# Kernel optimization log

Measured on AMD Instinct MI355X. Metric: run time of the kernel, lower is better.

The kernel has to match this reference:

```python
import jax, jax.numpy as jnp
import numpy as np

K_MASK = -2.3819763e+38
NUM_KV_HEADS = 4
SOFT_CAP = 50.0
WINDOW = 1024
ROPE_BASE = 10000.0
ROPE_SCALE = 1.0


def rms_norm(x, scale=None, eps=1e-6):
    var = jnp.mean(jnp.square(x), axis=-1, keepdims=True)
    normed = x * jax.lax.rsqrt(var + eps)
    if scale is not None:
        normed = normed * (1.0 + scale)
    return normed


def apply_rope(x, positions):
    # x: [B, T, N, H], positions: [B, T]
    head_dim = x.shape[-1]
    fraction = 2.0 * jnp.arange(head_dim // 2, dtype=jnp.float32) / head_dim
    timescale = ROPE_BASE ** fraction  # [H/2]
    sinusoid = positions[..., None, None].astype(jnp.float32) / timescale / ROPE_SCALE  # [B,T,1,H/2]
    sin, cos = jnp.sin(sinusoid), jnp.cos(sinusoid)
    first, second = jnp.split(x, 2, axis=-1)
    return jnp.concatenate([first * cos - second * sin,
                            second * cos + first * sin], axis=-1).astype(x.dtype)


def setup_inputs() -> dict:
    key = jax.random.key(0)
    ks = jax.random.split(key, 8)
    B, T, D, N, K, H, F = 2, 2048, 2048, 8, NUM_KV_HEADS, 256, 8192
    CACHE = 4096
    x = jax.random.normal(ks[0], (B, T, D), dtype=jnp.float32)
    segment_pos = jnp.broadcast_to(jnp.arange(T, dtype=jnp.int32)[None, :], (B, T))
    # causal mask over cache slots: after scatter, slot s (< T) holds position s; slots >= T are empty
    s_idx = jnp.arange(CACHE)
    t_idx = jnp.arange(T)
    attn_mask = (s_idx[None, :] <= t_idx[:, None]) & (s_idx[None, :] < T)
    attn_mask = jnp.broadcast_to(attn_mask[None], (B, T, CACHE))
    cache_k = jnp.zeros((B, CACHE, K, H), dtype=jnp.float32)
    cache_v = jnp.zeros((B, CACHE, K, H), dtype=jnp.float32)
    cache_positions = jnp.zeros((B, CACHE), dtype=jnp.int32)
    end_index = jnp.zeros((B,), dtype=jnp.int32)
    w_q = jax.random.normal(ks[1], (N, D, H), dtype=jnp.float32) * 0.02
    w_kv = jax.random.normal(ks[2], (2, K, D, H), dtype=jnp.float32) * 0.02
    w_attn_vec = jax.random.normal(ks[3], (N, H, D), dtype=jnp.float32) * 0.02
    w_gating = jax.random.normal(ks[4], (2, F, D), dtype=jnp.float32) * 0.02
    w_linear = jax.random.normal(ks[5], (F, D), dtype=jnp.float32) * 0.02
    return {
        'x': x, 'segment_pos': segment_pos, 'attn_mask': attn_mask,
        'cache_k': cache_k, 'cache_v': cache_v,
        'cache_positions': cache_positions, 'end_index': end_index,
        'w_q': w_q, 'w_kv': w_kv, 'w_attn_vec': w_attn_vec,
        'q_norm_scale': jnp.zeros((H,), dtype=jnp.float32),
        'k_norm_scale': jnp.zeros((H,), dtype=jnp.float32),
        'pre_attn_scale': jnp.zeros((D,), dtype=jnp.float32),
        'post_attn_scale': jnp.zeros((D,), dtype=jnp.float32),
        'pre_ffw_scale': jnp.zeros((D,), dtype=jnp.float32),
        'post_ffw_scale': jnp.zeros((D,), dtype=jnp.float32),
        'w_gating': w_gating, 'w_linear': w_linear,
        'skip_scale': jnp.ones((1,), dtype=jnp.float32),
    }


def reference(x, segment_pos, attn_mask, cache_k, cache_v, cache_positions, end_index,
              w_q, w_kv, w_attn_vec, q_norm_scale, k_norm_scale,
              pre_attn_scale, post_attn_scale, pre_ffw_scale, post_ffw_scale,
              w_gating, w_linear, skip_scale):
    B, T, D = x.shape
    cache_size = cache_v.shape[1]

    h = rms_norm(x, pre_attn_scale)

    # --- attention ---
    q = jnp.einsum('BTD,NDH->BTNH', h, w_q)
    q = rms_norm(q, q_norm_scale)
    q = apply_rope(q, segment_pos)

    k, v = jnp.einsum('BSD,CKDH->CBSKH', h, w_kv)
    k = rms_norm(k, k_norm_scale)
    v = rms_norm(v, None)
    k = apply_rope(k, segment_pos)

    # KV-cache scatter (ring-buffer indexing)
    idx = (end_index[:, None] + jnp.arange(T)[None, :]) % cache_size  # [B,T]
    bidx = jnp.arange(B)[:, None]
    v = cache_v.at[bidx, idx].set(v)              # [B,S,K,H]
    k = cache_k.at[bidx, idx].set(k)
    cache_pos = cache_positions.at[bidx, idx].set(segment_pos)  # [B,S]

    # GQA logits
    N, H = q.shape[2], q.shape[3]
    G = N // NUM_KV_HEADS
    qg = q.reshape(B, T, NUM_KV_HEADS, G, H)
    logits = jnp.einsum('BTKGH,BSKH->BTKGS', qg, k).reshape(B, T, N, cache_size)

    # soft cap
    logits = jnp.tanh(logits / SOFT_CAP) * SOFT_CAP

    # sliding-window mask against cache positions
    sliding = (cache_pos[:, None, :] > segment_pos[:, :, None] - WINDOW) & \
              (cache_pos[:, None, :] < segment_pos[:, :, None] + WINDOW)  # [B,T,S]
    mask = attn_mask & sliding

    padded = jnp.where(mask[:, :, None, :], logits, K_MASK)
    probs = jax.nn.softmax(padded, axis=-1).astype(k.dtype)

    pg = probs.reshape(B, T, NUM_KV_HEADS, G, cache_size)
    encoded = jnp.einsum('BTKGS,BSKH->BTKGH', pg, v).reshape(B, T, N, H)
    attn_out = jnp.einsum('BTNH,NHD->BTD', encoded, w_attn_vec)

    # post-attn norm + residual (skip_scale on the skip connection)
    attn_out = rms_norm(attn_out, post_attn_scale)
    attn_out = x * skip_scale + attn_out

    # --- feed-forward ---
    ffw_in = rms_norm(attn_out, pre_ffw_scale)
    gate = jnp.einsum('BTF,CHF->BTCH', ffw_in, w_gating)  # C=2
    act = jax.nn.gelu(gate[..., 0, :]) * gate[..., 1, :]
    ffw_out = jnp.einsum('BTH,HF->BTF', act, w_linear)
    ffw_out = rms_norm(ffw_out, post_ffw_scale)

    return attn_out + ffw_out
```

## Files before the change

kernel.cpp:

```cpp
#include <hip/hip_runtime.h>


typedef _Float16 h8 __attribute__((ext_vector_type(8)));
typedef _Float16 h4 __attribute__((ext_vector_type(4)));
typedef float f4 __attribute__((ext_vector_type(4)));

#define BDIM 2
#define TDIM 2048
#define DDIM 2048
#define NQ 8
#define NKV 4
#define HDIM 256
#define FDIM 8192
#define MROWS (BDIM * TDIM)
#define WINDOW 1024
#define QS 4096

#define BAR() asm volatile("s_barrier" ::: "memory")

__device__ __forceinline__ float gelu_fast(float x) {
  float u = 1.5957691216057308f * (x + 0.044715f * x * x * x);
  float e = __expf(u);
  return x * e / (e + 1.f);
}

__device__ __forceinline__ void g2l16(const _Float16* g, _Float16* l) {
  __builtin_amdgcn_global_load_lds(
      (const __attribute__((address_space(1))) void*)g,
      (__attribute__((address_space(3))) void*)l, 16, 0, 0);
}

__device__ inline float block_sum(float v, float* sbuf) {
#pragma unroll
  for (int off = 32; off; off >>= 1) v += __shfl_xor(v, off, 64);
  __syncthreads();
  if ((threadIdx.x & 63) == 0) sbuf[threadIdx.x >> 6] = v;
  __syncthreads();
  return sbuf[0] + sbuf[1] + sbuf[2] + sbuf[3];
}

template <int EPI>
__global__ __launch_bounds__(512, 2) void gemm256(
    const _Float16* __restrict__ A, const _Float16* __restrict__ Bt,
    void* __restrict__ Cout, int M, int Nc, int K) {
  __shared__ _Float16 As[3][256 * 64];
  __shared__ _Float16 Bs[3][128 * 64];
  (void)M;
  const int tid = threadIdx.x;
  const int lane = tid & 63, w = tid >> 6;
  const int nwg = gridDim.x;
  const int bid2 = (blockIdx.x & 7) * (nwg >> 3) + (blockIdx.x >> 3);
  const int nbx = Nc >> 7;
  const int bx = bid2 % nbx, by = bid2 / nbx;
  const int m0 = by * 256, n0 = bx * 128;
  const int wm = (w >> 1) * 64, wn = (w & 1) * 64;
  const int l16 = lane & 15, quad = lane >> 4;

  const int lr = lane >> 3;
  const int swz8 = ((lane & 7) ^ lr) << 3;
  const _Float16* Ag = A + (size_t)(m0 + w * 32 + lr) * K + swz8;
  const _Float16* Bg = Bt + (size_t)(n0 + w * 16 + lr) * K + swz8;

  const int qs8 = (quad ^ (l16 & 3)) << 3;
  const int kxo = ((l16 >> 2) & 1) << 5;
  int aoff[4], boff[4];
#pragma unroll
  for (int i = 0; i < 4; i++) {
    aoff[i] = (wm + i * 16 + l16) * 64 + qs8;
    boff[i] = (wn + i * 16 + l16) * 64 + qs8;
  }

  f4 acc[4][4];
#pragma unroll
  for (int i = 0; i < 4; i++)
#pragma unroll
    for (int j = 0; j < 4; j++) {
      acc[i][j][0] = 0.f; acc[i][j][1] = 0.f; acc[i][j][2] = 0.f; acc[i][j][3] = 0.f;
    }

#define SA(b, kt, c) g2l16(Ag + (size_t)(c) * 8 * K + (size_t)(kt) * 64, \
                           &As[b][(w * 32 + (c) * 8) * 64])
#define SB(b, kt, c) g2l16(Bg + (size_t)(c) * 8 * K + (size_t)(kt) * 64, \
                           &Bs[b][(w * 16 + (c) * 8) * 64])

  SA(0, 0, 0); SA(0, 0, 1); SA(0, 0, 2); SA(0, 0, 3); SB(0, 0, 0); SB(0, 0, 1);
  SA(1, 1, 0); SA(1, 1, 1); SA(1, 1, 2); SA(1, 1, 3); SB(1, 1, 0); SB(1, 1, 1);
  asm volatile("s_waitcnt vmcnt(6)" ::: "memory");
  BAR();

  const int nt = K >> 6;
  for (int kt = 0; kt < nt; ++kt) {
    const int cur = kt % 3, nb = (kt + 2) % 3;
    const bool pf = (kt + 2) < nt;
    const _Float16* Ab = As[cur];
    const _Float16* Bb = Bs[cur];
    h8 af[4][2], bf[4][2];
#pragma unroll
    for (int i = 0; i < 4; i++) {
      af[i][0] = *(const h8*)&Ab[aoff[i] + kxo];
      af[i][1] = *(const h8*)&Ab[aoff[i] + (kxo ^ 32)];
    }
#pragma unroll
    for (int i = 0; i < 2; i++) {
      bf[i][0] = *(const h8*)&Bb[boff[i] + kxo];
      bf[i][1] = *(const h8*)&Bb[boff[i] + (kxo ^ 32)];
    }
    if (pf) { SA(nb, kt + 2, 0); SA(nb, kt + 2, 1); SA(nb, kt + 2, 2); }
    BAR();
    __builtin_amdgcn_s_setprio(1);
#pragma unroll
    for (int mi = 0; mi < 4; mi++)
#pragma unroll
      for (int ni = 0; ni < 2; ni++)
#pragma unroll
        for (int ks = 0; ks < 2; ks++)
          acc[mi][ni] = __builtin_amdgcn_mfma_f32_16x16x32_f16(
              af[mi][ks], bf[ni][ks], acc[mi][ni], 0, 0, 0);
    __builtin_amdgcn_s_setprio(0);
    BAR();
#pragma unroll
    for (int i = 2; i < 4; i++) {
      bf[i][0] = *(const h8*)&Bb[boff[i] + kxo];
      bf[i][1] = *(const h8*)&Bb[boff[i] + (kxo ^ 32)];
    }
    if (pf) { SA(nb, kt + 2, 3); SB(nb, kt + 2, 0); SB(nb, kt + 2, 1); }
    BAR();
    __builtin_amdgcn_s_setprio(1);
#pragma unroll
    for (int mi = 0; mi < 4; mi++)
#pragma unroll
      for (int ni = 2; ni < 4; ni++)
#pragma unroll
        for (int ks = 0; ks < 2; ks++)
          acc[mi][ni] = __builtin_amdgcn_mfma_f32_16x16x32_f16(
              af[mi][ks], bf[ni][ks], acc[mi][ni], 0, 0, 0);
    __builtin_amdgcn_s_setprio(0);
    if (pf)                 asm volatile("s_waitcnt vmcnt(6)" ::: "memory");
    else if (kt + 2 == nt)  asm volatile("s_waitcnt vmcnt(0)" ::: "memory");
    BAR();
  }
#undef SA
#undef SB

#pragma unroll
  for (int mi = 0; mi < 4; mi++)
#pragma unroll
    for (int ni = 0; ni < 4; ni++)
#pragma unroll
      for (int r = 0; r < 4; r++) {
        const int rg = m0 + wm + mi * 16 + quad * 4 + r;
        const int cg = n0 + wn + ni * 16 + l16;
        const size_t idx = (size_t)rg * Nc + cg;
        if (EPI == 0) ((float*)Cout)[idx] = acc[mi][ni][r];
        else          ((_Float16*)Cout)[idx] = (_Float16)acc[mi][ni][r];
      }
}

__global__ __launch_bounds__(512, 2) void gemm_gate256(
    const _Float16* __restrict__ A, const _Float16* __restrict__ B0,
    const _Float16* __restrict__ B1, _Float16* __restrict__ act,
    int M, int Nc, int K) {
  __shared__ _Float16 As[3][256 * 64];
  __shared__ _Float16 B0s[3][64 * 64];
  __shared__ _Float16 B1s[3][64 * 64];
  (void)M;
  const int tid = threadIdx.x;
  const int lane = tid & 63, w = tid >> 6;
  const int nwg = gridDim.x;
  const int bid2 = (blockIdx.x & 7) * (nwg >> 3) + (blockIdx.x >> 3);
  const int nbx = Nc >> 6;
  const int bx = bid2 % nbx, by = bid2 / nbx;
  const int m0 = by * 256, n0 = bx * 64;
  const int wm = (w >> 1) * 64, wn = (w & 1) * 32;
  const int l16 = lane & 15, quad = lane >> 4;

  const int lr = lane >> 3;
  const int swz8 = ((lane & 7) ^ lr) << 3;
  const _Float16* Ag  = A  + (size_t)(m0 + w * 32 + lr) * K + swz8;
  const _Float16* B0g = B0 + (size_t)(n0 + w * 8 + lr) * K + swz8;
  const _Float16* B1g = B1 + (size_t)(n0 + w * 8 + lr) * K + swz8;

  const int qs8 = (quad ^ (l16 & 3)) << 3;
  const int kxo = ((l16 >> 2) & 1) << 5;
  int aoff[4], boff[2];
#pragma unroll
  for (int i = 0; i < 4; i++) aoff[i] = (wm + i * 16 + l16) * 64 + qs8;
#pragma unroll
  for (int i = 0; i < 2; i++) boff[i] = (wn + i * 16 + l16) * 64 + qs8;

  f4 acc0[4][2], acc1[4][2];
#pragma unroll
  for (int i = 0; i < 4; i++)
#pragma unroll
    for (int j = 0; j < 2; j++) {
      acc0[i][j][0] = 0.f; acc0[i][j][1] = 0.f; acc0[i][j][2] = 0.f; acc0[i][j][3] = 0.f;
      acc1[i][j][0] = 0.f; acc1[i][j][1] = 0.f; acc1[i][j][2] = 0.f; acc1[i][j][3] = 0.f;
    }

#define SA(b, kt, c) g2l16(Ag + (size_t)(c) * 8 * K + (size_t)(kt) * 64, \
                           &As[b][(w * 32 + (c) * 8) * 64])
#define SB0(b, kt) g2l16(B0g + (size_t)(kt) * 64, &B0s[b][w * 8 * 64])
#define SB1(b, kt) g2l16(B1g + (size_t)(kt) * 64, &B1s[b][w * 8 * 64])

  SA(0, 0, 0); SA(0, 0, 1); SA(0, 0, 2); SA(0, 0, 3); SB0(0, 0); SB1(0, 0);
  SA(1, 1, 0); SA(1, 1, 1); SA(1, 1, 2); SA(1, 1, 3); SB0(1, 1); SB1(1, 1);
  asm volatile("s_waitcnt vmcnt(6)" ::: "memory");
  BAR();

  const int nt = K >> 6;
  for (int kt = 0; kt < nt; ++kt) {
    const int cur = kt % 3, nb = (kt + 2) % 3;
    const bool pf = (kt + 2) < nt;
    const _Float16* Ab = As[cur];
    const _Float16* Bb0 = B0s[cur];
    const _Float16* Bb1 = B1s[cur];
    h8 af[4][2], b0f[2][2], b1f[2][2];
#pragma unroll
    for (int i = 0; i < 4; i++) {
      af[i][0] = *(const h8*)&Ab[aoff[i] + kxo];
      af[i][1] = *(const h8*)&Ab[aoff[i] + (kxo ^ 32)];
    }
#pragma unroll
    for (int i = 0; i < 2; i++) {
      b0f[i][0] = *(const h8*)&Bb0[boff[i] + kxo];
      b0f[i][1] = *(const h8*)&Bb0[boff[i] + (kxo ^ 32)];
    }
    if (pf) { SA(nb, kt + 2, 0); SA(nb, kt + 2, 1); SA(nb, kt + 2, 2); }
    BAR();
    __builtin_amdgcn_s_setprio(1);
#pragma unroll
    for (int mi = 0; mi < 4; mi++)
#pragma unroll
      for (int ni = 0; ni < 2; ni++)
#pragma unroll
        for (int ks = 0; ks < 2; ks++)
          acc0[mi][ni] = __builtin_amdgcn_mfma_f32_16x16x32_f16(
              af[mi][ks], b0f[ni][ks], acc0[mi][ni], 0, 0, 0);
    __builtin_amdgcn_s_setprio(0);
    BAR();
#pragma unroll
    for (int i = 0; i < 2; i++) {
      b1f[i][0] = *(const h8*)&Bb1[boff[i] + kxo];
      b1f[i][1] = *(const h8*)&Bb1[boff[i] + (kxo ^ 32)];
    }
    if (pf) { SA(nb, kt + 2, 3); SB0(nb, kt + 2); SB1(nb, kt + 2); }
    BAR();
    __builtin_amdgcn_s_setprio(1);
#pragma unroll
    for (int mi = 0; mi < 4; mi++)
#pragma unroll
      for (int ni = 0; ni < 2; ni++)
#pragma unroll
        for (int ks = 0; ks < 2; ks++)
          acc1[mi][ni] = __builtin_amdgcn_mfma_f32_16x16x32_f16(
              af[mi][ks], b1f[ni][ks], acc1[mi][ni], 0, 0, 0);
    __builtin_amdgcn_s_setprio(0);
    if (pf)                 asm volatile("s_waitcnt vmcnt(6)" ::: "memory");
    else if (kt + 2 == nt)  asm volatile("s_waitcnt vmcnt(0)" ::: "memory");
    BAR();
  }
#undef SA
#undef SB0
#undef SB1

#pragma unroll
  for (int mi = 0; mi < 4; mi++)
#pragma unroll
    for (int ni = 0; ni < 2; ni++)
#pragma unroll
      for (int r = 0; r < 4; r++) {
        const int rg = m0 + wm + mi * 16 + quad * 4 + r;
        const int cg = n0 + wn + ni * 16 + l16;
        act[(size_t)rg * Nc + cg] =
            (_Float16)(gelu_fast(acc0[mi][ni][r]) * acc1[mi][ni][r]);
      }
}

__global__ __launch_bounds__(256) void transpose_cast_kernel(
    const float* __restrict__ in, _Float16* __restrict__ out,
    int R, int C, size_t in_zstride, size_t out_zstride) {
  __shared__ float tile[64][65];
  const float* ip = in + blockIdx.z * in_zstride;
  _Float16* op = out + blockIdx.z * out_zstride;
  const int cb = blockIdx.x * 64, rb = blockIdx.y * 64;
  const int tx = threadIdx.x & 15, ty = threadIdx.x >> 4;
#pragma unroll
  for (int i = 0; i < 4; i++) {
    f4 v = *(const f4*)&ip[(size_t)(rb + ty + 16 * i) * C + cb + tx * 4];
    tile[ty + 16 * i][tx * 4 + 0] = v[0];
    tile[ty + 16 * i][tx * 4 + 1] = v[1];
    tile[ty + 16 * i][tx * 4 + 2] = v[2];
    tile[ty + 16 * i][tx * 4 + 3] = v[3];
  }
  __syncthreads();
#pragma unroll
  for (int i = 0; i < 4; i++) {
    const int c = ty + 16 * i;
    h4 o;
#pragma unroll
    for (int j = 0; j < 4; j++) o[j] = (_Float16)tile[tx * 4 + j][c];
    *(h4*)&op[(size_t)(cb + c) * R + rb + tx * 4] = o;
  }
}

__global__ void cast_fp16_kernel(const float* __restrict__ in,
                                 _Float16* __restrict__ out, int n4) {
  int i = blockIdx.x * 256 + threadIdx.x;
  if (i < n4) {
    f4 v = ((const f4*)in)[i];
    h4 o;
    o[0] = (_Float16)v[0]; o[1] = (_Float16)v[1];
    o[2] = (_Float16)v[2]; o[3] = (_Float16)v[3];
    ((h4*)out)[i] = o;
  }
}

__global__ __launch_bounds__(256) void rmsnorm_fp16_kernel(
    const float* __restrict__ in, const float* __restrict__ scale,
    _Float16* __restrict__ out) {
  __shared__ float sbuf[4];
  const int row = blockIdx.x, tid = threadIdx.x;
  const float* r = in + (size_t)row * 2048;
  f4 a = ((const f4*)r)[tid];
  f4 b = ((const f4*)r)[tid + 256];
  float ss = a[0]*a[0] + a[1]*a[1] + a[2]*a[2] + a[3]*a[3] +
             b[0]*b[0] + b[1]*b[1] + b[2]*b[2] + b[3]*b[3];
  float tot = block_sum(ss, sbuf);
  float rs = rsqrtf(tot * (1.f / 2048.f) + 1e-6f);
  f4 s0 = ((const f4*)scale)[tid];
  f4 s1 = ((const f4*)scale)[tid + 256];
  h4 o0, o1;
#pragma unroll
  for (int j = 0; j < 4; j++) {
    o0[j] = (_Float16)(a[j] * rs * (1.f + s0[j]));
    o1[j] = (_Float16)(b[j] * rs * (1.f + s1[j]));
  }
  ((h4*)(out + (size_t)row * 2048))[tid] = o0;
  ((h4*)(out + (size_t)row * 2048))[tid + 256] = o1;
}

__global__ __launch_bounds__(256) void headnorm_qkv_kernel(
    const _Float16* __restrict__ qkv, _Float16* __restrict__ out,
    const float* __restrict__ qsc, const float* __restrict__ ksc,
    const int* __restrict__ pos_arr) {
  const int inst = blockIdx.x * 4 + (threadIdx.x >> 6);
  const int lane = threadIdx.x & 63;
  const int row = inst >> 4, slot = inst & 15;
  const _Float16* r = qkv + (size_t)row * QS + slot * 256;
  h4 vh = ((const h4*)r)[lane];
  f4 v;
#pragma unroll
  for (int j = 0; j < 4; j++) v[j] = (float)vh[j];
  float ss = v[0]*v[0] + v[1]*v[1] + v[2]*v[2] + v[3]*v[3];
#pragma unroll
  for (int off = 32; off; off >>= 1) ss += __shfl_xor(ss, off, 64);
  const float rs = rsqrtf(ss * (1.f / 256.f) + 1e-6f);
  const float* scale = (slot < 8) ? qsc : (slot < 12 ? ksc : nullptr);
  f4 nv;
  if (scale) {
    f4 sc = ((const f4*)scale)[lane];
#pragma unroll
    for (int j = 0; j < 4; j++) nv[j] = v[j] * rs * (1.f + sc[j]);
  } else {
#pragma unroll
    for (int j = 0; j < 4; j++) nv[j] = v[j] * rs;
  }
  h4 res;
  if (slot < 12) {
    const float pos = (float)pos_arr[row];
    const bool lo = lane < 32;
#pragma unroll
    for (int j = 0; j < 4; j++) {
      float partner = __shfl_xor(nv[j], 32, 64);
      const int ph = (lane * 4 + j) & 127;
      float it = exp2f((float)ph * -0.103810253f);
      float ang = pos * it;
      float sn, cs;
      sincosf(ang, &sn, &cs);
      res[j] = (_Float16)(lo ? (nv[j] * cs - partner * sn)
                             : (nv[j] * cs + partner * sn));
    }
  } else {
#pragma unroll
    for (int j = 0; j < 4; j++) res[j] = (_Float16)nv[j];
  }
  ((h4*)(out + (size_t)row * QS + slot * 256))[lane] = res;
}

__global__ __launch_bounds__(256) void transpose_v_kernel(
    const _Float16* __restrict__ qkvh, _Float16* __restrict__ vT) {
  __shared__ _Float16 tile[32][33];
  const int z = blockIdx.z;
  const int b = z >> 2, kvh = z & 3;
  const int tb = blockIdx.x * 32, hb = blockIdx.y * 32;
  const int x = threadIdx.x, y = threadIdx.y;
#pragma unroll
  for (int i = 0; i < 4; i++)
    tile[y + 8 * i][x] =
        qkvh[(size_t)(b * TDIM + tb + y + 8 * i) * QS + 3072 + kvh * 256 + hb + x];
  __syncthreads();
#pragma unroll
  for (int i = 0; i < 4; i++)
    vT[((size_t)z * HDIM + hb + y + 8 * i) * TDIM + tb + x] = tile[x][y + 8 * i];
}

__global__ __launch_bounds__(256) void attn_kernel(
    const _Float16* __restrict__ qkvh, const _Float16* __restrict__ vT,
    _Float16* __restrict__ enc) {
  __shared__ _Float16 Ks[32 * 256];
  __shared__ _Float16 Vs[256 * 32];
  __shared__ _Float16 Ps[4][16 * 32];
  const int t0 = blockIdx.x * 64;
  const int n = blockIdx.y;
  const int b = blockIdx.z;
  const int kvh = n >> 1;
  const int tid = threadIdx.x;
  const int w = tid >> 6, lane = tid & 63, l16 = lane & 15, quad = lane >> 4;
  const int kxr = (l16 >> 2) & 1;
  const int qsK8 = (quad ^ (l16 & 3)) << 3;
  const int qsV8 = (quad ^ ((l16 >> 1) & 3)) << 3;

  h8 qfrag[8];
  {
    const int trow = t0 + w * 16 + l16;
    const _Float16* qp =
        qkvh + (size_t)(b * TDIM + trow) * QS + n * HDIM + quad * 8;
#pragma unroll
    for (int ks = 0; ks < 8; ks++) qfrag[ks] = *(const h8*)(qp + ks * 32);
  }

  f4 O[16];
#pragma unroll
  for (int i = 0; i < 16; i++) { O[i][0] = 0.f; O[i][1] = 0.f; O[i][2] = 0.f; O[i][3] = 0.f; }
  float m_i[4], l_i[4];
#pragma unroll
  for (int r = 0; r < 4; r++) { m_i[r] = -1e30f; l_i[r] = 0.f; }

  int s_begin = t0 - (WINDOW - 1);
  if (s_begin < 0) s_begin = 0;
  s_begin &= ~31;
  const int s_end = t0 + 64;
  const _Float16* kbase = qkvh + (size_t)b * TDIM * QS + 2048 + kvh * HDIM;
  const _Float16* vbase = vT + ((size_t)(b * NKV + kvh) * HDIM) * TDIM;

  for (int s0 = s_begin; s0 < s_end; s0 += 32) {
    __syncthreads();
#pragma unroll
    for (int p = 0; p < 4; p++) {
      int g = p * 256 + tid;
      {
        int si = g >> 5, c = g & 31;
        *(h8*)&Ks[si * 256 + ((c ^ (si & 7)) << 3)] =
            *(const h8*)(kbase + (size_t)(s0 + si) * QS + (c << 3));
      }
      {
        int h = g >> 2, c = g & 3;
        *(h8*)&Vs[h * 32 + ((c ^ ((g >> 3) & 3)) << 3)] =
            *(const h8*)(vbase + (size_t)h * TDIM + s0 + (c << 3));
      }
    }
    __syncthreads();

    float P[2][4], cmax[4];
#pragma unroll
    for (int r = 0; r < 4; r++) cmax[r] = -1e30f;
#pragma unroll
    for (int sc = 0; sc < 2; sc++) {
      f4 lg; lg[0] = 0.f; lg[1] = 0.f; lg[2] = 0.f; lg[3] = 0.f;
#pragma unroll
      for (int ks = 0; ks < 8; ks++) {
        h8 kb = *(const h8*)&Ks[(sc * 16 + l16) * 256 + ((ks ^ kxr) << 5) + qsK8];
        lg = __builtin_amdgcn_mfma_f32_16x16x32_f16(qfrag[ks], kb, lg, 0, 0, 0);
      }
      const int scol = s0 + sc * 16 + l16;
#pragma unroll
      for (int r = 0; r < 4; r++) {
        const int trow = t0 + w * 16 + quad * 4 + r;
        float t = __expf(lg[r] * 0.04f);
        float xv = 50.f - 100.f * __builtin_amdgcn_rcpf(t + 1.f);
        bool valid = (scol <= trow) && (scol > trow - WINDOW);
        P[sc][r] = valid ? xv : -1e30f;
        cmax[r] = fmaxf(cmax[r], P[sc][r]);
      }
    }
#pragma unroll
    for (int off = 1; off < 16; off <<= 1)
#pragma unroll
      for (int r = 0; r < 4; r++) cmax[r] = fmaxf(cmax[r], __shfl_xor(cmax[r], off, 16));
    float alpha[4], psum[4];
#pragma unroll
    for (int r = 0; r < 4; r++) {
      float mnew = fmaxf(m_i[r], cmax[r]);
      alpha[r] = __expf(m_i[r] - mnew);
      m_i[r] = mnew;
      psum[r] = 0.f;
    }
#pragma unroll
    for (int sc = 0; sc < 2; sc++)
#pragma unroll
      for (int r = 0; r < 4; r++) {
        float pv = __expf(P[sc][r] - m_i[r]);
        P[sc][r] = pv;
        psum[r] += pv;
      }
#pragma unroll
    for (int off = 1; off < 16; off <<= 1)
#pragma unroll
      for (int r = 0; r < 4; r++) psum[r] += __shfl_xor(psum[r], off, 16);
#pragma unroll
    for (int r = 0; r < 4; r++) l_i[r] = l_i[r] * alpha[r] + psum[r];
#pragma unroll
    for (int i = 0; i < 16; i++)
#pragma unroll
      for (int r = 0; r < 4; r++) O[i][r] *= alpha[r];
#pragma unroll
    for (int sc = 0; sc < 2; sc++)
#pragma unroll
      for (int r = 0; r < 4; r++)
        Ps[w][(quad * 4 + r) * 32 + sc * 16 + l16] = (_Float16)P[sc][r];
    h8 pa = *(const h8*)&Ps[w][l16 * 32 + quad * 8];
#pragma unroll
    for (int ht = 0; ht < 16; ht++) {
      h8 vb = *(const h8*)&Vs[(ht * 16 + l16) * 32 + qsV8];
      O[ht] = __builtin_amdgcn_mfma_f32_16x16x32_f16(pa, vb, O[ht], 0, 0, 0);
    }
  }

  float invl[4];
#pragma unroll
  for (int r = 0; r < 4; r++) invl[r] = 1.f / l_i[r];
#pragma unroll
  for (int ht = 0; ht < 16; ht++)
#pragma unroll
    for (int r = 0; r < 4; r++) {
      const int trow = t0 + w * 16 + quad * 4 + r;
      enc[((size_t)(b * TDIM + trow)) * (NQ * HDIM) + n * HDIM + ht * 16 + l16] =
          (_Float16)(O[ht][r] * invl[r]);
    }
}

__global__ __launch_bounds__(256) void postattn_kernel(
    const float* __restrict__ attnraw, const float* __restrict__ x,
    const float* __restrict__ post_scale, const float* __restrict__ pre_ffw_scale,
    const float* __restrict__ skip, float* __restrict__ attn_out,
    _Float16* __restrict__ ffw_in) {
  __shared__ float sbuf[4];
  const int row = blockIdx.x, tid = threadIdx.x;
  const float* ar = attnraw + (size_t)row * 2048;
  const float* xr = x + (size_t)row * 2048;
  f4 a0 = ((const f4*)ar)[tid], a1 = ((const f4*)ar)[tid + 256];
  float ss = a0[0]*a0[0] + a0[1]*a0[1] + a0[2]*a0[2] + a0[3]*a0[3] +
             a1[0]*a1[0] + a1[1]*a1[1] + a1[2]*a1[2] + a1[3]*a1[3];
  float tot = block_sum(ss, sbuf);
  float rs = rsqrtf(tot * (1.f / 2048.f) + 1e-6f);
  const float sk = skip[0];
  f4 x0 = ((const f4*)xr)[tid], x1 = ((const f4*)xr)[tid + 256];
  f4 p0 = ((const f4*)post_scale)[tid], p1 = ((const f4*)post_scale)[tid + 256];
  f4 at0, at1;
#pragma unroll
  for (int j = 0; j < 4; j++) {
    at0[j] = x0[j] * sk + a0[j] * rs * (1.f + p0[j]);
    at1[j] = x1[j] * sk + a1[j] * rs * (1.f + p1[j]);
  }
  ((f4*)(attn_out + (size_t)row * 2048))[tid] = at0;
  ((f4*)(attn_out + (size_t)row * 2048))[tid + 256] = at1;
  float ss2 = at0[0]*at0[0] + at0[1]*at0[1] + at0[2]*at0[2] + at0[3]*at0[3] +
              at1[0]*at1[0] + at1[1]*at1[1] + at1[2]*at1[2] + at1[3]*at1[3];
  float tot2 = block_sum(ss2, sbuf);
  float rs2 = rsqrtf(tot2 * (1.f / 2048.f) + 1e-6f);
  f4 f0 = ((const f4*)pre_ffw_scale)[tid], f1 = ((const f4*)pre_ffw_scale)[tid + 256];
  h4 o0, o1;
#pragma unroll
  for (int j = 0; j < 4; j++) {
    o0[j] = (_Float16)(at0[j] * rs2 * (1.f + f0[j]));
    o1[j] = (_Float16)(at1[j] * rs2 * (1.f + f1[j]));
  }
  ((h4*)(ffw_in + (size_t)row * 2048))[tid] = o0;
  ((h4*)(ffw_in + (size_t)row * 2048))[tid + 256] = o1;
}

__global__ __launch_bounds__(256) void final_kernel(
    const _Float16* __restrict__ ffw, const float* __restrict__ attn_out,
    const float* __restrict__ post_ffw_scale, float* __restrict__ out) {
  __shared__ float sbuf[4];
  const int row = blockIdx.x, tid = threadIdx.x;
  const _Float16* fr = ffw + (size_t)row * 2048;
  const float* ar = attn_out + (size_t)row * 2048;
  h4 fh0 = ((const h4*)fr)[tid], fh1 = ((const h4*)fr)[tid + 256];
  f4 a0, a1;
#pragma unroll
  for (int j = 0; j < 4; j++) { a0[j] = (float)fh0[j]; a1[j] = (float)fh1[j]; }
  float ss = a0[0]*a0[0] + a0[1]*a0[1] + a0[2]*a0[2] + a0[3]*a0[3] +
             a1[0]*a1[0] + a1[1]*a1[1] + a1[2]*a1[2] + a1[3]*a1[3];
  float tot = block_sum(ss, sbuf);
  float rs = rsqrtf(tot * (1.f / 2048.f) + 1e-6f);
  f4 s0 = ((const f4*)post_ffw_scale)[tid], s1 = ((const f4*)post_ffw_scale)[tid + 256];
  f4 x0 = ((const f4*)ar)[tid], x1 = ((const f4*)ar)[tid + 256];
  f4 o0, o1;
#pragma unroll
  for (int j = 0; j < 4; j++) {
    o0[j] = x0[j] + a0[j] * rs * (1.f + s0[j]);
    o1[j] = x1[j] + a1[j] * rs * (1.f + s1[j]);
  }
  ((f4*)(out + (size_t)row * 2048))[tid] = o0;
  ((f4*)(out + (size_t)row * 2048))[tid + 256] = o1;
}

extern "C" void kernel_launch(void* const* d_in, const int* in_sizes, int n_in,
                              void* d_out, int out_size, void* d_ws, size_t ws_size,
                              hipStream_t stream) {
  (void)in_sizes; (void)n_in; (void)out_size; (void)ws_size;
  const float* x              = (const float*)d_in[0];
  const int*   segment_pos    = (const int*)d_in[1];
  const float* w_q            = (const float*)d_in[7];
  const float* w_kv           = (const float*)d_in[8];
  const float* w_attn_vec     = (const float*)d_in[9];
  const float* q_norm_scale   = (const float*)d_in[10];
  const float* k_norm_scale   = (const float*)d_in[11];
  const float* pre_attn_scale = (const float*)d_in[12];
  const float* post_attn_scale= (const float*)d_in[13];
  const float* pre_ffw_scale  = (const float*)d_in[14];
  const float* post_ffw_scale = (const float*)d_in[15];
  const float* w_gating       = (const float*)d_in[16];
  const float* w_linear       = (const float*)d_in[17];
  const float* skip_scale     = (const float*)d_in[18];

  char* ws = (char*)d_ws;
  const size_t MB = 1024 * 1024;
  _Float16* Wqkv  = (_Float16*)(ws + 0);
  _Float16* Wo    = (_Float16*)(ws + 0);
  _Float16* Wg    = (_Float16*)(ws + 0);
  _Float16* Wl    = (_Float16*)(ws + 0);
  _Float16* Hbf   = (_Float16*)(ws + 64 * MB);
  float* attnF    = (float*)(ws + 80 * MB);
  _Float16* qkvraw= (_Float16*)(ws + 112 * MB);
  _Float16* qkvh  = (_Float16*)(ws + 144 * MB);
  _Float16* enc   = (_Float16*)(ws + 176 * MB);
  float* attnraw  = (float*)(ws + 192 * MB);
  _Float16* vT    = (_Float16*)(ws + 224 * MB);
  _Float16* act   = (_Float16*)(ws + 112 * MB);
  _Float16* ffw   = (_Float16*)(ws + 192 * MB);
  float* outp     = (float*)d_out;

  transpose_cast_kernel<<<dim3(HDIM / 64, DDIM / 64, NQ), 256, 0, stream>>>(
      w_q, Wqkv, DDIM, HDIM, (size_t)DDIM * HDIM, (size_t)HDIM * DDIM);
  transpose_cast_kernel<<<dim3(HDIM / 64, DDIM / 64, NKV), 256, 0, stream>>>(
      w_kv, Wqkv + (size_t)2048 * DDIM, DDIM, HDIM,
      (size_t)DDIM * HDIM, (size_t)HDIM * DDIM);
  transpose_cast_kernel<<<dim3(HDIM / 64, DDIM / 64, NKV), 256, 0, stream>>>(
      w_kv + (size_t)NKV * DDIM * HDIM, Wqkv + (size_t)3072 * DDIM, DDIM, HDIM,
      (size_t)DDIM * HDIM, (size_t)HDIM * DDIM);
  rmsnorm_fp16_kernel<<<MROWS, 256, 0, stream>>>(x, pre_attn_scale, Hbf);
  gemm256<1><<<dim3((QS / 128) * (MROWS / 256)), 512, 0, stream>>>(
      Hbf, Wqkv, qkvraw, MROWS, QS, DDIM);
  headnorm_qkv_kernel<<<(MROWS * 16) / 4, 256, 0, stream>>>(
      qkvraw, qkvh, q_norm_scale, k_norm_scale, segment_pos);
  transpose_v_kernel<<<dim3(TDIM / 32, HDIM / 32, BDIM * NKV), dim3(32, 8), 0, stream>>>(
      qkvh, vT);
  attn_kernel<<<dim3(TDIM / 64, NQ, BDIM), 256, 0, stream>>>(qkvh, vT, enc);
  transpose_cast_kernel<<<dim3(DDIM / 64, (NQ * HDIM) / 64, 1), 256, 0, stream>>>(
      w_attn_vec, Wo, NQ * HDIM, DDIM, 0, 0);
  gemm256<0><<<dim3((DDIM / 128) * (MROWS / 256)), 512, 0, stream>>>(
      enc, Wo, attnraw, MROWS, DDIM, NQ * HDIM);
  postattn_kernel<<<MROWS, 256, 0, stream>>>(attnraw, x, post_attn_scale,
                                             pre_ffw_scale, skip_scale, attnF, Hbf);
  cast_fp16_kernel<<<(2 * FDIM * DDIM / 4 + 255) / 256, 256, 0, stream>>>(
      w_gating, Wg, 2 * FDIM * DDIM / 4);
  gemm_gate256<<<dim3((FDIM / 64) * (MROWS / 256)), 512, 0, stream>>>(
      Hbf, Wg, Wg + (size_t)FDIM * DDIM, act, MROWS, FDIM, DDIM);
  transpose_cast_kernel<<<dim3(DDIM / 64, FDIM / 64, 1), 256, 0, stream>>>(
      w_linear, Wl, FDIM, DDIM, 0, 0);
  gemm256<1><<<dim3((DDIM / 128) * (MROWS / 256)), 512, 0, stream>>>(
      act, Wl, ffw, MROWS, DDIM, FDIM);
  final_kernel<<<MROWS, 256, 0, stream>>>(ffw, attnF, post_ffw_scale, outp);
}
```

Measured before the change: 1.159 ms.

## Widen gate GEMM tile to 256x128 with double buffering and column-major block order

The fused gate/up GEMM tile grows from 256x64 to 256x128 per block. Each wave now computes 64x64 outputs per branch, which doubles the accumulators and halves how often the A tile is reloaded. The pipeline drops from three stages to two, with all next-tile loads issued in one batch followed by a full vmcnt(0) wait. Block order now walks the M dimension first, so blocks sharing weight columns run together. The cost is higher register pressure at launch bounds (512,2) and less latency hiding from the shallower pipeline.

```diff
diff --git a/kernel.cpp b/kernel.cpp
--- a/kernel.cpp
+++ b/kernel.cpp
@@ -160,78 +160,84 @@
     const _Float16* __restrict__ A, const _Float16* __restrict__ B0,
     const _Float16* __restrict__ B1, _Float16* __restrict__ act,
     int M, int Nc, int K) {
-  __shared__ _Float16 As[3][256 * 64];
-  __shared__ _Float16 B0s[3][64 * 64];
-  __shared__ _Float16 B1s[3][64 * 64];
-  (void)M;
+  __shared__ _Float16 As[2][256 * 64];
+  __shared__ _Float16 B0s[2][128 * 64];
+  __shared__ _Float16 B1s[2][128 * 64];
   const int tid = threadIdx.x;
   const int lane = tid & 63, w = tid >> 6;
   const int nwg = gridDim.x;
   const int bid2 = (blockIdx.x & 7) * (nwg >> 3) + (blockIdx.x >> 3);
-  const int nbx = Nc >> 6;
-  const int bx = bid2 % nbx, by = bid2 / nbx;
-  const int m0 = by * 256, n0 = bx * 64;
-  const int wm = (w >> 1) * 64, wn = (w & 1) * 32;
+  const int nby = M >> 8;
+  const int by = bid2 % nby, bx = bid2 / nby;
+  const int m0 = by * 256, n0 = bx * 128;
+  const int wm = (w >> 1) * 64, wn = (w & 1) * 64;
   const int l16 = lane & 15, quad = lane >> 4;
 
   const int lr = lane >> 3;
   const int swz8 = ((lane & 7) ^ lr) << 3;
   const _Float16* Ag  = A  + (size_t)(m0 + w * 32 + lr) * K + swz8;
-  const _Float16* B0g = B0 + (size_t)(n0 + w * 8 + lr) * K + swz8;
-  const _Float16* B1g = B1 + (size_t)(n0 + w * 8 + lr) * K + swz8;
+  const _Float16* B0g = B0 + (size_t)(n0 + w * 16 + lr) * K + swz8;
+  const _Float16* B1g = B1 + (size_t)(n0 + w * 16 + lr) * K + swz8;
 
   const int qs8 = (quad ^ (l16 & 3)) << 3;
   const int kxo = ((l16 >> 2) & 1) << 5;
-  int aoff[4], boff[2];
-#pragma unroll
-  for (int i = 0; i < 4; i++) aoff[i] = (wm + i * 16 + l16) * 64 + qs8;
-#pragma unroll
-  for (int i = 0; i < 2; i++) boff[i] = (wn + i * 16 + l16) * 64 + qs8;
-
-  f4 acc0[4][2], acc1[4][2];
+  int aoff[4], boff[4];
+#pragma unroll
+  for (int i = 0; i < 4; i++) {
+    aoff[i] = (wm + i * 16 + l16) * 64 + qs8;
+    boff[i] = (wn + i * 16 + l16) * 64 + qs8;
+  }
+
+  f4 acc0[4][4], acc1[4][4];
 #pragma unroll
   for (int i = 0; i < 4; i++)
 #pragma unroll
-    for (int j = 0; j < 2; j++) {
+    for (int j = 0; j < 4; j++) {
       acc0[i][j][0] = 0.f; acc0[i][j][1] = 0.f; acc0[i][j][2] = 0.f; acc0[i][j][3] = 0.f;
       acc1[i][j][0] = 0.f; acc1[i][j][1] = 0.f; acc1[i][j][2] = 0.f; acc1[i][j][3] = 0.f;
     }
 
-#define SA(b, kt, c) g2l16(Ag + (size_t)(c) * 8 * K + (size_t)(kt) * 64, \
-                           &As[b][(w * 32 + (c) * 8) * 64])
-#define SB0(b, kt) g2l16(B0g + (size_t)(kt) * 64, &B0s[b][w * 8 * 64])
-#define SB1(b, kt) g2l16(B1g + (size_t)(kt) * 64, &B1s[b][w * 8 * 64])
-
-  SA(0, 0, 0); SA(0, 0, 1); SA(0, 0, 2); SA(0, 0, 3); SB0(0, 0); SB1(0, 0);
-  SA(1, 1, 0); SA(1, 1, 1); SA(1, 1, 2); SA(1, 1, 3); SB0(1, 1); SB1(1, 1);
-  asm volatile("s_waitcnt vmcnt(6)" ::: "memory");
+#define SA(b, kt, c)  g2l16(Ag  + (size_t)(c) * 8 * K + (size_t)(kt) * 64, \
+                            &As[b][(w * 32 + (c) * 8) * 64])
+#define SB0(b, kt, c) g2l16(B0g + (size_t)(c) * 8 * K + (size_t)(kt) * 64, \
+                            &B0s[b][(w * 16 + (c) * 8) * 64])
+#define SB1(b, kt, c) g2l16(B1g + (size_t)(c) * 8 * K + (size_t)(kt) * 64, \
+                            &B1s[b][(w * 16 + (c) * 8) * 64])
+
+  SA(0, 0, 0); SA(0, 0, 1); SA(0, 0, 2); SA(0, 0, 3);
+  SB0(0, 0, 0); SB0(0, 0, 1); SB1(0, 0, 0); SB1(0, 0, 1);
+  asm volatile("s_waitcnt vmcnt(0)" ::: "memory");
   BAR();
 
   const int nt = K >> 6;
   for (int kt = 0; kt < nt; ++kt) {
-    const int cur = kt % 3, nb = (kt + 2) % 3;
-    const bool pf = (kt + 2) < nt;
-    const _Float16* Ab = As[cur];
+    const int cur = kt & 1, nb = cur ^ 1;
+    const bool pf = (kt + 1) < nt;
+    const _Float16* Ab  = As[cur];
     const _Float16* Bb0 = B0s[cur];
     const _Float16* Bb1 = B1s[cur];
-    h8 af[4][2], b0f[2][2], b1f[2][2];
+    h8 af[4][2], b0f[4][2], b1f[4][2];
 #pragma unroll
     for (int i = 0; i < 4; i++) {
       af[i][0] = *(const h8*)&Ab[aoff[i] + kxo];
       af[i][1] = *(const h8*)&Ab[aoff[i] + (kxo ^ 32)];
     }
 #pragma unroll
-    for (int i = 0; i < 2; i++) {
+    for (int i = 0; i < 4; i++) {
       b0f[i][0] = *(const h8*)&Bb0[boff[i] + kxo];
       b0f[i][1] = *(const h8*)&Bb0[boff[i] + (kxo ^ 32)];
     }
-    if (pf) { SA(nb, kt + 2, 0); SA(nb, kt + 2, 1); SA(nb, kt + 2, 2); }
+    if (pf) {
+      SA(nb, kt + 1, 0); SA(nb, kt + 1, 1); SA(nb, kt + 1, 2); SA(nb, kt + 1, 3);
+      SB0(nb, kt + 1, 0); SB0(nb, kt + 1, 1);
+      SB1(nb, kt + 1, 0); SB1(nb, kt + 1, 1);
+    }
     BAR();
     __builtin_amdgcn_s_setprio(1);
 #pragma unroll
     for (int mi = 0; mi < 4; mi++)
 #pragma unroll
-      for (int ni = 0; ni < 2; ni++)
+      for (int ni = 0; ni < 4; ni++)
 #pragma unroll
         for (int ks = 0; ks < 2; ks++)
           acc0[mi][ni] = __builtin_amdgcn_mfma_f32_16x16x32_f16(
@@ -239,24 +245,22 @@
     __builtin_amdgcn_s_setprio(0);
     BAR();
 #pragma unroll
-    for (int i = 0; i < 2; i++) {
+    for (int i = 0; i < 4; i++) {
       b1f[i][0] = *(const h8*)&Bb1[boff[i] + kxo];
       b1f[i][1] = *(const h8*)&Bb1[boff[i] + (kxo ^ 32)];
     }
-    if (pf) { SA(nb, kt + 2, 3); SB0(nb, kt + 2); SB1(nb, kt + 2); }
     BAR();
     __builtin_amdgcn_s_setprio(1);
 #pragma unroll
     for (int mi = 0; mi < 4; mi++)
 #pragma unroll
-      for (int ni = 0; ni < 2; ni++)
+      for (int ni = 0; ni < 4; ni++)
 #pragma unroll
         for (int ks = 0; ks < 2; ks++)
           acc1[mi][ni] = __builtin_amdgcn_mfma_f32_16x16x32_f16(
               af[mi][ks], b1f[ni][ks], acc1[mi][ni], 0, 0, 0);
     __builtin_amdgcn_s_setprio(0);
-    if (pf)                 asm volatile("s_waitcnt vmcnt(6)" ::: "memory");
-    else if (kt + 2 == nt)  asm volatile("s_waitcnt vmcnt(0)" ::: "memory");
+    if (pf) asm volatile("s_waitcnt vmcnt(0)" ::: "memory");
     BAR();
   }
 #undef SA
@@ -266,7 +270,7 @@
 #pragma unroll
   for (int mi = 0; mi < 4; mi++)
 #pragma unroll
-    for (int ni = 0; ni < 2; ni++)
+    for (int ni = 0; ni < 4; ni++)
 #pragma unroll
       for (int r = 0; r < 4; r++) {
         const int rg = m0 + wm + mi * 16 + quad * 4 + r;
@@ -666,7 +670,7 @@
                                              pre_ffw_scale, skip_scale, attnF, Hbf);
   cast_fp16_kernel<<<(2 * FDIM * DDIM / 4 + 255) / 256, 256, 0, stream>>>(
       w_gating, Wg, 2 * FDIM * DDIM / 4);
-  gemm_gate256<<<dim3((FDIM / 64) * (MROWS / 256)), 512, 0, stream>>>(
+  gemm_gate256<<<dim3((FDIM / 128) * (MROWS / 256)), 512, 0, stream>>>(
       Hbf, Wg, Wg + (size_t)FDIM * DDIM, act, MROWS, FDIM, DDIM);
   transpose_cast_kernel<<<dim3(DDIM / 64, FDIM / 64, 1), 256, 0, stream>>>(
       w_linear, Wl, FDIM, DDIM, 0, 0);
```

Result: no change. 1.147 ms (-1.0%).
